# Performance work log

Hardware: AMD Instinct MI355X
Metric: run time of the kernel (lower is better)

The kernel has to match this reference:

```python
import jax, jax.numpy as jnp
import numpy as np

B, L, D, H, DK = 2, 1024, 1024, 16, 64
LN_EPS = 1e-5


def setup_inputs() -> dict:
    key = jax.random.key(0)
    ks = jax.random.split(key, 4)
    x = jax.random.normal(ks[0], (B, L, D), dtype=jnp.float32)
    W_qkv = jax.random.normal(ks[1], (D, 3 * D), dtype=jnp.float32) * 0.02
    W_o = jax.random.normal(ks[2], (D, D), dtype=jnp.float32) * 0.02
    W_LTM = jax.random.normal(ks[3], (H, DK, DK), dtype=jnp.float32) * 0.5
    return {
        "x": x,
        "W_qkv": W_qkv,
        "W_o": W_o,
        "W_LTM": W_LTM,
        "V_gs": jnp.zeros((H,), jnp.float32),
        "V_T0": jnp.zeros((H,), jnp.float32),
        "beta_tau": jnp.ones((H,), jnp.float32),
        "beta_gm": jnp.ones((H,), jnp.float32) * 0.1,
        "C_ch": jnp.ones((H,), jnp.float32),
        "gamma": jnp.ones((H,), jnp.float32) * 0.1,
        "alpha_ppd": jnp.ones((1,), jnp.float32),
        "IC_threshold": jnp.ones((1,), jnp.float32),
        "gate": jnp.zeros((H,), jnp.float32),
    }


def _stp_physics(W_LTM, V_gs, V_T0, beta_tau, beta_gm, C_ch, alpha_ppd, IC_threshold):
    # per-head params broadcast to (H, dk, dk)
    V_eff = V_gs[:, None, None] - V_T0[:, None, None] + W_LTM  # U_T = 1.0
    sp = jax.nn.softplus(V_eff)
    g_ch = beta_tau[:, None, None] * sp
    retention = jnp.exp(-g_ch / C_ch[:, None, None])  # = 1 - Lambda
    G = beta_gm[:, None, None] * sp * jax.nn.sigmoid(V_eff)
    sign_mask = jnp.tanh(alpha_ppd * (g_ch - IC_threshold))
    return retention, G, sign_mask


def reference(x, W_qkv, W_o, W_LTM, V_gs, V_T0, beta_tau, beta_gm, C_ch,
              gamma, alpha_ppd, IC_threshold, gate):
    Bb, Ll, Dd = x.shape
    qkv = (x @ W_qkv).reshape(Bb, Ll, 3, H, DK)
    q, k, v = qkv[:, :, 0], qkv[:, :, 1], qkv[:, :, 2]  # (B,L,H,dk)

    # LayerNorm over dk, no affine
    mu = jnp.mean(k, axis=-1, keepdims=True)
    var = jnp.var(k, axis=-1, keepdims=True)
    k_normed = (k - mu) * jax.lax.rsqrt(var + LN_EPS)

    # ---- causal softmax attention ----
    scale = 1.0 / np.sqrt(DK)
    attn = jnp.einsum('bihd,bjhd->bhij', q, k) * scale
    causal = jnp.tril(jnp.ones((Ll, Ll), dtype=bool))
    attn = jnp.where(causal[None, None], attn, -jnp.inf)
    attn = jax.nn.softmax(attn, axis=-1)
    softmax_out = jnp.einsum('bhij,bjhd->bihd', attn, v)  # (B,L,H,dk)

    # ---- STP fast-weight recurrence ----
    retention, G, sign_mask = _stp_physics(W_LTM, V_gs, V_T0, beta_tau,
                                           beta_gm, C_ch, alpha_ppd, IC_threshold)
    coeff = gamma[:, None, None] * sign_mask * G  # (H,dk,dk)

    def step(F_state, qkv_t):
        q_t, k_t, v_t = qkv_t  # (B,H,dk) each; k_t is normed
        hebbian = jnp.einsum('bhd,bhe->bhde', v_t, k_t)
        F_new = retention[None] * F_state + coeff[None] * hebbian
        y_t = jnp.einsum('bhde,bhe->bhd', W_LTM[None] + F_new, q_t)
        return F_new, y_t

    xs = (jnp.moveaxis(q, 1, 0), jnp.moveaxis(k_normed, 1, 0), jnp.moveaxis(v, 1, 0))
    F0 = jnp.zeros((Bb, H, DK, DK), dtype=x.dtype)
    _, ys = jax.lax.scan(step, F0, xs)
    stp_out = jnp.moveaxis(ys, 0, 1)  # (B,L,H,dk)

    g = jax.nn.sigmoid(gate)[None, None, :, None]
    y = g * softmax_out + (1.0 - g) * stp_out
    y = y.reshape(Bb, Ll, Dd)
    return y @ W_o
```

## Files before the change

kernel.cpp:

```cpp
#include <hip/hip_runtime.h>
#include <hip/hip_bf16.h>
#include <math.h>

#define LQ 1024
#define DH 1024
#define NH 16
#define DKH 64

typedef __bf16 bf16x8 __attribute__((ext_vector_type(8)));
typedef float f32x4 __attribute__((ext_vector_type(4)));
typedef const unsigned int __attribute__((address_space(1)))* gas1_t;
typedef unsigned int __attribute__((address_space(3)))* las3_t;

__device__ __forceinline__ unsigned pack2bf(float a, float b) {
  union { __hip_bfloat16 h[2]; unsigned u; } t;
  t.h[0] = __float2bfloat16(a);
  t.h[1] = __float2bfloat16(b);
  return t.u;
}
__device__ __forceinline__ void store_c(float* p, float v) { *p = v; }
__device__ __forceinline__ void store_c(__hip_bfloat16* p, float v) { *p = __float2bfloat16(v); }

__global__ __launch_bounds__(256) void physics_kernel(
    const float* __restrict__ W_LTM, const float* __restrict__ V_gs, const float* __restrict__ V_T0,
    const float* __restrict__ beta_tau, const float* __restrict__ beta_gm, const float* __restrict__ C_ch,
    const float* __restrict__ gamma_, const float* __restrict__ alpha_ppd, const float* __restrict__ IC_thr,
    const float* __restrict__ gate, float* __restrict__ ret, float* __restrict__ ret64,
    float* __restrict__ co, float* __restrict__ g_out) {
  int idx = blockIdx.x * 256 + threadIdx.x;
  int h = idx >> 12;
  float w = W_LTM[idx];
  float veff = V_gs[h] - V_T0[h] + w;
  float sp = fmaxf(veff, 0.f) + log1pf(expf(-fabsf(veff)));
  float gch = beta_tau[h] * sp;
  float e1 = gch / C_ch[h];
  float retv = expf(-e1);
  float sig = 1.f / (1.f + expf(-veff));
  float G = beta_gm[h] * sp * sig;
  float sm = tanhf(alpha_ppd[0] * (gch - IC_thr[0]));
  ret[idx] = retv;
  ret64[idx] = expf(-64.f * e1);
  co[idx] = gamma_[h] * sm * G;
  if (idx < NH) g_out[idx] = 1.f / (1.f + expf(-gate[idx]));
}

__global__ __launch_bounds__(256) void cvt_kernel(const float* __restrict__ in, __hip_bfloat16* __restrict__ out) {
  size_t i = (size_t)(blockIdx.x * 256 + threadIdx.x) * 4;
  float4 v = *(const float4*)(in + i);
  __hip_bfloat16 t[4] = {__float2bfloat16(v.x), __float2bfloat16(v.y),
                         __float2bfloat16(v.z), __float2bfloat16(v.w)};
  *(uint2*)(out + i) = *(uint2*)t;
}

__global__ __launch_bounds__(256) void tcvt_kernel(const float* __restrict__ W, __hip_bfloat16* __restrict__ Wt,
                                                   int K, int N) {
  __shared__ float t[32][33];
  int n0 = blockIdx.x * 32, k0 = blockIdx.y * 32;
  int r = threadIdx.x >> 5, c = threadIdx.x & 31;
#pragma unroll
  for (int i = 0; i < 4; i++) t[r + 8 * i][c] = W[(size_t)(k0 + r + 8 * i) * N + n0 + c];
  __syncthreads();
#pragma unroll
  for (int i = 0; i < 4; i++)
    Wt[(size_t)(n0 + r + 8 * i) * K + k0 + c] = __float2bfloat16(t[c][r + 8 * i]);
}

__global__ __launch_bounds__(256) void mix_kernel(const float* __restrict__ so, const float* __restrict__ stp,
                                                  const float* __restrict__ g, __hip_bfloat16* __restrict__ out) {
  size_t base = (size_t)(blockIdx.x * 256 + threadIdx.x) * 4;
  float gv = g[(base >> 6) & 15];
  float4 a = *(const float4*)(so + base);
  float4 b = *(const float4*)(stp + base);
  __hip_bfloat16 t[4] = {__float2bfloat16(gv * a.x + (1.f - gv) * b.x),
                         __float2bfloat16(gv * a.y + (1.f - gv) * b.y),
                         __float2bfloat16(gv * a.z + (1.f - gv) * b.z),
                         __float2bfloat16(gv * a.w + (1.f - gv) * b.w)};
  *(uint2*)(out + base) = *(uint2*)t;
}

template <typename OT>
__global__ __launch_bounds__(256) void gemm_bt_kernel(
    const __hip_bfloat16* __restrict__ A, const __hip_bfloat16* __restrict__ Bt,
    OT* __restrict__ C, int M, int N, int K) {
  __shared__ unsigned short As[128 * 32];
  __shared__ unsigned short Bs[128 * 32];
  const int tid = threadIdx.x;
  const int w = tid >> 6, lane = tid & 63;
  const int quad = lane >> 4, l16 = lane & 15;
  const int wm = w & 1, wn = w >> 1;
  const int row0 = blockIdx.y * 128, col0 = blockIdx.x * 128;
  const int sr = lane >> 2;
  const int sk = (lane & 3) * 8;
  f32x4 acc[4][4];
#pragma unroll
  for (int i = 0; i < 4; i++)
#pragma unroll
    for (int j = 0; j < 4; j++) acc[i][j] = (f32x4){0.f, 0.f, 0.f, 0.f};

  for (int k0 = 0; k0 < K; k0 += 32) {
    __syncthreads();
#pragma unroll
    for (int c = 0; c < 2; c++) {
      int s = c * 4 + w;
      const __hip_bfloat16* gA = A + (size_t)(row0 + s * 16 + sr) * K + k0 + sk;
      __builtin_amdgcn_global_load_lds((gas1_t)gA, (las3_t)((char*)As + s * 1024), 16, 0, 0);
      const __hip_bfloat16* gB = Bt + (size_t)(col0 + s * 16 + sr) * K + k0 + sk;
      __builtin_amdgcn_global_load_lds((gas1_t)gB, (las3_t)((char*)Bs + s * 1024), 16, 0, 0);
    }
    __syncthreads();
    bf16x8 af[4], bfr[4];
#pragma unroll
    for (int i = 0; i < 4; i++)
      af[i] = *(const bf16x8*)((const char*)As + (((wm * 64 + i * 16 + l16) * 32 + quad * 8) << 1));
#pragma unroll
    for (int j = 0; j < 4; j++)
      bfr[j] = *(const bf16x8*)((const char*)Bs + (((wn * 64 + j * 16 + l16) * 32 + quad * 8) << 1));
#pragma unroll
    for (int i = 0; i < 4; i++)
#pragma unroll
      for (int j = 0; j < 4; j++)
        acc[i][j] = __builtin_amdgcn_mfma_f32_16x16x32_bf16(af[i], bfr[j], acc[i][j], 0, 0, 0);
  }
#pragma unroll
  for (int i = 0; i < 4; i++) {
    int rowb = row0 + wm * 64 + i * 16 + quad * 4;
#pragma unroll
    for (int j = 0; j < 4; j++) {
      int col = col0 + wn * 64 + j * 16 + l16;
#pragma unroll
      for (int r = 0; r < 4; r++)
        store_c(&C[(size_t)(rowb + r) * N + col], acc[i][j][r]);
    }
  }
}

__global__ __launch_bounds__(256) void cvt_qkv_kernel(
    const __hip_bfloat16* __restrict__ qkvb, __hip_bfloat16* __restrict__ vt, float* __restrict__ kn) {
  const int tc = blockIdx.x, h = blockIdx.y, b = blockIdx.z;
  const int bh = b * NH + h;
  const int tid = threadIdx.x;
  const int r = tid >> 2;
  const int q4 = tid & 3;
  const int t = tc * 64 + r;
  __shared__ float Ls[64][65];
  const size_t rowbase = (size_t)(b * LQ + t) * 3 * DH + h * DKH + q4 * 16;

  {
    bf16x8 k0 = *(const bf16x8*)(qkvb + rowbase + DH);
    bf16x8 k1 = *(const bf16x8*)(qkvb + rowbase + DH + 8);
    float vv[16];
#pragma unroll
    for (int i = 0; i < 8; i++) { vv[i] = (float)k0[i]; vv[8 + i] = (float)k1[i]; }
    float s1 = 0.f, s2 = 0.f;
#pragma unroll
    for (int i = 0; i < 16; i++) { s1 += vv[i]; s2 += vv[i] * vv[i]; }
    s1 += __shfl_xor(s1, 1); s2 += __shfl_xor(s2, 1);
    s1 += __shfl_xor(s1, 2); s2 += __shfl_xor(s2, 2);
    float mu = s1 * (1.f / 64.f);
    float var = s2 * (1.f / 64.f) - mu * mu;
    float inv = rsqrtf(var + 1e-5f);
    float* kdst = kn + ((size_t)(b * LQ + t) * NH + h) * DKH + q4 * 16;
#pragma unroll
    for (int i4 = 0; i4 < 4; i4++) {
      float4 c = {(vv[i4 * 4] - mu) * inv, (vv[i4 * 4 + 1] - mu) * inv,
                  (vv[i4 * 4 + 2] - mu) * inv, (vv[i4 * 4 + 3] - mu) * inv};
      *(float4*)(kdst + i4 * 4) = c;
    }
  }
  {
    bf16x8 v0 = *(const bf16x8*)(qkvb + rowbase + 2 * DH);
    bf16x8 v1 = *(const bf16x8*)(qkvb + rowbase + 2 * DH + 8);
#pragma unroll
    for (int i = 0; i < 8; i++) {
      Ls[r][q4 * 16 + i] = (float)v0[i];
      Ls[r][q4 * 16 + 8 + i] = (float)v1[i];
    }
  }
  __syncthreads();
  {
    const int dr = tid >> 2, tq = tid & 3;
    __hip_bfloat16 o[16];
#pragma unroll
    for (int i = 0; i < 16; i++) o[i] = __float2bfloat16(Ls[tq * 16 + i][dr]);
    __hip_bfloat16* dst = vt + ((size_t)bh * DKH + dr) * LQ + tc * 64 + tq * 16;
    *(uint4*)dst = *(uint4*)o;
    *(uint4*)(dst + 8) = *(uint4*)(o + 8);
  }
}

__global__ __launch_bounds__(256) void attn_mfma_kernel(
    const __hip_bfloat16* __restrict__ qkvb, const __hip_bfloat16* __restrict__ vt,
    float* __restrict__ so) {
  const int it = 15 - blockIdx.x;
  const int h = blockIdx.y, b = blockIdx.z;
  const int bh = b * NH + h;
  const int tid = threadIdx.x;
  const int w = tid >> 6, lane = tid & 63;
  const int l16 = lane & 15, quad = lane >> 4;
  __shared__ __attribute__((aligned(16))) __hip_bfloat16 Ks[8 * 64 * 8];
  __shared__ __attribute__((aligned(16))) __hip_bfloat16 Vs[8 * 64 * 8];
  const int i0 = it * 64;
  const int q_abs = i0 + w * 16 + l16;
  bf16x8 aq[2];
  aq[0] = *(const bf16x8*)(qkvb + (size_t)(b * LQ + q_abs) * 3 * DH + h * DKH + quad * 8);
  aq[1] = *(const bf16x8*)(qkvb + (size_t)(b * LQ + q_abs) * 3 * DH + h * DKH + 32 + quad * 8);
  f32x4 o[4];
#pragma unroll
  for (int dt = 0; dt < 4; dt++) o[dt] = (f32x4){0.f, 0.f, 0.f, 0.f};
  float mrun = -3e38f, lrun = 0.f;

  for (int jt = 0; jt <= it; jt++) {
    const int j0 = jt * 64;
    __syncthreads();
#pragma unroll
    for (int ff = 0; ff < 2; ff++) {
      const int f = w * 2 + ff;
      const int nt = f >> 1, kk = f & 1;
      const __hip_bfloat16* gk = qkvb + (size_t)(b * LQ + j0 + nt * 16 + l16) * 3 * DH + DH +
                                 h * DKH + kk * 32 + quad * 8;
      __builtin_amdgcn_global_load_lds((gas1_t)gk, (las3_t)(Ks + f * 512), 16, 0, 0);
      const __hip_bfloat16* gv = vt + ((size_t)bh * DKH + nt * 16 + l16) * LQ + j0 + kk * 32 + quad * 8;
      __builtin_amdgcn_global_load_lds((gas1_t)gv, (las3_t)(Vs + f * 512), 16, 0, 0);
    }
    __syncthreads();
    f32x4 s[4];
#pragma unroll
    for (int nt = 0; nt < 4; nt++) s[nt] = (f32x4){0.f, 0.f, 0.f, 0.f};
#pragma unroll
    for (int kk = 0; kk < 2; kk++)
#pragma unroll
      for (int nt = 0; nt < 4; nt++) {
        bf16x8 bk = *(const bf16x8*)(Ks + ((nt * 2 + kk) * 64 + lane) * 8);
        s[nt] = __builtin_amdgcn_mfma_f32_16x16x32_bf16(bk, aq[kk], s[nt], 0, 0, 0);
      }
#pragma unroll
    for (int nt = 0; nt < 4; nt++)
#pragma unroll
      for (int r = 0; r < 4; r++) {
        float sv = s[nt][r] * 0.125f;
        if (jt == it && (j0 + nt * 16 + quad * 4 + r > q_abs)) sv = -1e30f;
        s[nt][r] = sv;
      }
    float mx = -3e38f;
#pragma unroll
    for (int nt = 0; nt < 4; nt++)
#pragma unroll
      for (int r = 0; r < 4; r++) mx = fmaxf(mx, s[nt][r]);
    mx = fmaxf(mx, __shfl_xor(mx, 16));
    mx = fmaxf(mx, __shfl_xor(mx, 32));
    float mn = fmaxf(mrun, mx);
    float al = __expf(mrun - mn);
    mrun = mn;
    float p[4][4];
    float rs = 0.f;
#pragma unroll
    for (int nt = 0; nt < 4; nt++)
#pragma unroll
      for (int r = 0; r < 4; r++) {
        float pv = __expf(s[nt][r] - mn);
        p[nt][r] = pv;
        rs += pv;
      }
    rs += __shfl_xor(rs, 16);
    rs += __shfl_xor(rs, 32);
    lrun = lrun * al + rs;
    unsigned pk[4][2];
#pragma unroll
    for (int nt = 0; nt < 4; nt++) {
      pk[nt][0] = pack2bf(p[nt][0], p[nt][1]);
      pk[nt][1] = pack2bf(p[nt][2], p[nt][3]);
    }
    const int srcA = l16 | ((quad & 1) << 5);
    const bool hi_sel = (quad >> 1) != 0;
    bf16x8 ap[2];
#pragma unroll
    for (int kk = 0; kk < 2; kk++) {
      union { unsigned u[4]; bf16x8 v; } cv;
#pragma unroll
      for (int g = 0; g < 2; g++) {
        int src = srcA + (g << 4);
        unsigned lo0 = (unsigned)__shfl((int)pk[kk * 2][0], src);
        unsigned lo1 = (unsigned)__shfl((int)pk[kk * 2][1], src);
        unsigned hi0 = (unsigned)__shfl((int)pk[kk * 2 + 1][0], src);
        unsigned hi1 = (unsigned)__shfl((int)pk[kk * 2 + 1][1], src);
        cv.u[g * 2] = hi_sel ? hi0 : lo0;
        cv.u[g * 2 + 1] = hi_sel ? hi1 : lo1;
      }
      ap[kk] = cv.v;
    }
#pragma unroll
    for (int dt = 0; dt < 4; dt++)
#pragma unroll
      for (int r = 0; r < 4; r++) o[dt][r] *= al;
#pragma unroll
    for (int kk = 0; kk < 2; kk++)
#pragma unroll
      for (int dt = 0; dt < 4; dt++) {
        bf16x8 bv = *(const bf16x8*)(Vs + ((dt * 2 + kk) * 64 + lane) * 8);
        o[dt] = __builtin_amdgcn_mfma_f32_16x16x32_bf16(bv, ap[kk], o[dt], 0, 0, 0);
      }
  }
  float inv = 1.f / lrun;
  float* ob = so + ((size_t)(b * LQ + q_abs) * NH + h) * DKH + quad * 4;
#pragma unroll
  for (int dt = 0; dt < 4; dt++) {
    float4 c = {o[dt][0] * inv, o[dt][1] * inv, o[dt][2] * inv, o[dt][3] * inv};
    *(float4*)(ob + dt * 16) = c;
  }
}

__global__ __launch_bounds__(256) void state_kernel(
    const __hip_bfloat16* __restrict__ qkvb, const float* __restrict__ kn,
    const float* __restrict__ ret_g, const float* __restrict__ co_g, float* __restrict__ S) {
  const int bh = blockIdx.x >> 1;
  const int half = blockIdx.x & 1;
  const int c = blockIdx.y;
  const int bb = bh >> 4, h = bh & 15;
  const int tid = threadIdx.x;
  const int dl = tid >> 3, j = tid & 7;
  const int d = half * 32 + dl;
  float F[8], R[8], Cc[8];
  const int base = h * 4096 + d * 64 + j * 8;
#pragma unroll
  for (int i = 0; i < 8; i++) {
    F[i] = 0.f;
    R[i] = ret_g[base + i];
    Cc[i] = co_g[base + i];
  }
  __shared__ float kb[2][8][64], vb[2][8][64];
  const int t00 = c * 64;
  {
    float ld[4];
#pragma unroll
    for (int i = 0; i < 4; i++) {
      int idx = tid + 256 * i;
      int which = idx >> 9, rem = idx & 511, s = rem >> 6, e = rem & 63;
      int t = t00 + s;
      if (which == 0) ld[i] = kn[((size_t)(bb * LQ + t) * NH + h) * DKH + e];
      else            ld[i] = __bfloat162float(qkvb[((size_t)(bb * LQ + t) * 3 + 2) * DH + h * DKH + e]);
    }
#pragma unroll
    for (int i = 0; i < 4; i++) {
      int idx = tid + 256 * i;
      int which = idx >> 9, rem = idx & 511, s = rem >> 6, e = rem & 63;
      if (which == 0) kb[0][s][e] = ld[i];
      else            vb[0][s][e] = ld[i];
    }
  }
  __syncthreads();
  for (int sc = 0; sc < 8; sc++) {
    const int p = sc & 1;
    float l2[4];
    if (sc < 7) {
      int t0 = t00 + (sc + 1) * 8;
#pragma unroll
      for (int i = 0; i < 4; i++) {
        int idx = tid + 256 * i;
        int which = idx >> 9, rem = idx & 511, s = rem >> 6, e = rem & 63;
        int t = t0 + s;
        if (which == 0) l2[i] = kn[((size_t)(bb * LQ + t) * NH + h) * DKH + e];
        else            l2[i] = __bfloat162float(qkvb[((size_t)(bb * LQ + t) * 3 + 2) * DH + h * DKH + e]);
      }
    }
#pragma unroll
    for (int s = 0; s < 8; s++) {
      float vd = vb[p][s][d];
#pragma unroll
      for (int i = 0; i < 8; i++) {
        float ke = kb[p][s][j * 8 + i];
        F[i] = fmaf(Cc[i] * vd, ke, R[i] * F[i]);
      }
    }
    if (sc < 7) {
      const int pn = p ^ 1;
#pragma unroll
      for (int i = 0; i < 4; i++) {
        int idx = tid + 256 * i;
        int which = idx >> 9, rem = idx & 511, s = rem >> 6, e = rem & 63;
        if (which == 0) kb[pn][s][e] = l2[i];
        else            vb[pn][s][e] = l2[i];
      }
    }
    __syncthreads();
  }
  const size_t sb = ((size_t)c * 2048 + ((size_t)bb * 16 + h) * 64 + d) * 64 + j * 8;
#pragma unroll
  for (int i = 0; i < 8; i++) S[sb + i] = F[i];
}

__global__ __launch_bounds__(256) void combine_kernel(
    const float* __restrict__ S, const float* __restrict__ ret64, float* __restrict__ Fs) {
  int n = blockIdx.x * 256 + threadIdx.x;
  float r64 = ret64[n & 65535];
  float F = 0.f;
  Fs[n] = 0.f;
#pragma unroll
  for (int c = 1; c < 16; c++) {
    F = fmaf(r64, F, S[(size_t)(c - 1) * 131072 + n]);
    Fs[(size_t)c * 131072 + n] = F;
  }
}

__global__ __launch_bounds__(256) void scan_out_kernel(
    const __hip_bfloat16* __restrict__ qkvb, const float* __restrict__ kn, const float* __restrict__ W_LTM,
    const float* __restrict__ ret_g, const float* __restrict__ co_g, const float* __restrict__ Fs,
    float* __restrict__ stp) {
  const int bh = blockIdx.x >> 1;
  const int half = blockIdx.x & 1;
  const int c = blockIdx.y;
  const int bb = bh >> 4, h = bh & 15;
  const int tid = threadIdx.x;
  const int dl = tid >> 3, j = tid & 7;
  const int d = half * 32 + dl;
  float F[8], R[8], Cc[8], W[8];
  const int base = h * 4096 + d * 64 + j * 8;
  const size_t nbase = (size_t)c * 131072 + (((size_t)bb * 16 + h) * 64 + d) * 64 + j * 8;
#pragma unroll
  for (int i = 0; i < 8; i++) {
    F[i] = Fs[nbase + i];
    R[i] = ret_g[base + i];
    Cc[i] = co_g[base + i];
    W[i] = W_LTM[base + i];
  }
  __shared__ float qb[2][8][64], kb[2][8][64], vb[2][8][64];
  const int t00 = c * 64;
  {
    float ld[6];
#pragma unroll
    for (int i = 0; i < 6; i++) {
      int idx = tid + 256 * i;
      int which = idx >> 9, rem = idx & 511, s = rem >> 6, e = rem & 63;
      int t = t00 + s;
      if (which == 0)      ld[i] = __bfloat162float(qkvb[((size_t)(bb * LQ + t) * 3 + 0) * DH + h * DKH + e]);
      else if (which == 1) ld[i] = kn[((size_t)(bb * LQ + t) * NH + h) * DKH + e];
      else                 ld[i] = __bfloat162float(qkvb[((size_t)(bb * LQ + t) * 3 + 2) * DH + h * DKH + e]);
    }
#pragma unroll
    for (int i = 0; i < 6; i++) {
      int idx = tid + 256 * i;
      int which = idx >> 9, rem = idx & 511, s = rem >> 6, e = rem & 63;
      if (which == 0) qb[0][s][e] = ld[i];
      else if (which == 1) kb[0][s][e] = ld[i];
      else vb[0][s][e] = ld[i];
    }
  }
  __syncthreads();
  for (int sc = 0; sc < 8; sc++) {
    const int p = sc & 1;
    float l2[6];
    if (sc < 7) {
      int t0 = t00 + (sc + 1) * 8;
#pragma unroll
      for (int i = 0; i < 6; i++) {
        int idx = tid + 256 * i;
        int which = idx >> 9, rem = idx & 511, s = rem >> 6, e = rem & 63;
        int t = t0 + s;
        if (which == 0)      l2[i] = __bfloat162float(qkvb[((size_t)(bb * LQ + t) * 3 + 0) * DH + h * DKH + e]);
        else if (which == 1) l2[i] = kn[((size_t)(bb * LQ + t) * NH + h) * DKH + e];
        else                 l2[i] = __bfloat162float(qkvb[((size_t)(bb * LQ + t) * 3 + 2) * DH + h * DKH + e]);
      }
    }
#pragma unroll
    for (int s = 0; s < 8; s++) {
      float vd = vb[p][s][d];
      float yp = 0.f;
#pragma unroll
      for (int i = 0; i < 8; i++) {
        float ke = kb[p][s][j * 8 + i];
        F[i] = fmaf(Cc[i] * vd, ke, R[i] * F[i]);
        yp = fmaf(W[i] + F[i], qb[p][s][j * 8 + i], yp);
      }
      yp += __shfl_xor(yp, 1);
      yp += __shfl_xor(yp, 2);
      yp += __shfl_xor(yp, 4);
      if (j == 0) stp[((size_t)(bb * LQ + t00 + sc * 8 + s) * NH + h) * DKH + d] = yp;
    }
    if (sc < 7) {
      const int pn = p ^ 1;
#pragma unroll
      for (int i = 0; i < 6; i++) {
        int idx = tid + 256 * i;
        int which = idx >> 9, rem = idx & 511, s = rem >> 6, e = rem & 63;
        if (which == 0) qb[pn][s][e] = l2[i];
        else if (which == 1) kb[pn][s][e] = l2[i];
        else vb[pn][s][e] = l2[i];
      }
    }
    __syncthreads();
  }
}

extern "C" void kernel_launch(void* const* d_in, const int* in_sizes, int n_in,
                              void* d_out, int out_size, void* d_ws, size_t ws_size,
                              hipStream_t stream) {
  (void)in_sizes; (void)n_in; (void)out_size; (void)ws_size;
  const float* x        = (const float*)d_in[0];
  const float* W_qkv    = (const float*)d_in[1];
  const float* W_o      = (const float*)d_in[2];
  const float* W_LTM    = (const float*)d_in[3];
  const float* V_gs     = (const float*)d_in[4];
  const float* V_T0     = (const float*)d_in[5];
  const float* beta_tau = (const float*)d_in[6];
  const float* beta_gm  = (const float*)d_in[7];
  const float* C_ch     = (const float*)d_in[8];
  const float* gamma_   = (const float*)d_in[9];
  const float* alpha_p  = (const float*)d_in[10];
  const float* IC_thr   = (const float*)d_in[11];
  const float* gate     = (const float*)d_in[12];

  float* ws  = (float*)d_ws;
  __hip_bfloat16* qkvb = (__hip_bfloat16*)ws;
  float* kn    = ws + 3145728;
  float* so    = kn + 2097152;
  float* stp   = so + 2097152;
  float* ret   = stp + 2097152;
  float* ret64 = ret + 65536;
  float* co    = ret64 + 65536;
  float* g     = co + 65536;
  __hip_bfloat16* xb  = (__hip_bfloat16*)(g + 64);
  __hip_bfloat16* wot = xb + 2097152;
  float* Sbuf = (float*)(wot + 1048576);
  float* Fs   = Sbuf + 1966080;
  __hip_bfloat16* vtb = (__hip_bfloat16*)(Fs + 2097152);
  __hip_bfloat16* mixb = xb;
  __hip_bfloat16* wqt  = (__hip_bfloat16*)stp;
  float* out = (float*)d_out;

  physics_kernel<<<256, 256, 0, stream>>>(W_LTM, V_gs, V_T0, beta_tau, beta_gm, C_ch,
                                          gamma_, alpha_p, IC_thr, gate, ret, ret64, co, g);
  cvt_kernel<<<2048, 256, 0, stream>>>(x, xb);
  tcvt_kernel<<<dim3(96, 32), 256, 0, stream>>>(W_qkv, wqt, 1024, 3072);
  tcvt_kernel<<<dim3(32, 32), 256, 0, stream>>>(W_o, wot, 1024, 1024);
  gemm_bt_kernel<__hip_bfloat16><<<dim3(24, 16), 256, 0, stream>>>(xb, wqt, qkvb, 2048, 3072, 1024);
  cvt_qkv_kernel<<<dim3(16, 16, 2), 256, 0, stream>>>(qkvb, vtb, kn);
  attn_mfma_kernel<<<dim3(16, 16, 2), 256, 0, stream>>>(qkvb, vtb, so);
  state_kernel<<<dim3(64, 15), 256, 0, stream>>>(qkvb, kn, ret, co, Sbuf);
  combine_kernel<<<512, 256, 0, stream>>>(Sbuf, ret64, Fs);
  scan_out_kernel<<<dim3(64, 16), 256, 0, stream>>>(qkvb, kn, W_LTM, ret, co, Fs, stp);
  mix_kernel<<<2048, 256, 0, stream>>>(so, stp, g, mixb);
  gemm_bt_kernel<float><<<dim3(8, 16), 256, 0, stream>>>(mixb, wot, out, 2048, 1024, 1024);
}
```

Before: 241.0 us.

## Fuse prep kernels, fold mix into scan, halve scan chunks, store bf16 intermediates

```diff
diff --git a/kernel.cpp b/kernel.cpp
--- a/kernel.cpp
+++ b/kernel.cpp
@@ -21,61 +21,58 @@
 __device__ __forceinline__ void store_c(float* p, float v) { *p = v; }
 __device__ __forceinline__ void store_c(__hip_bfloat16* p, float v) { *p = __float2bfloat16(v); }
 
-__global__ __launch_bounds__(256) void physics_kernel(
+__global__ __launch_bounds__(256) void prep_kernel(
+    const float* __restrict__ x, const float* __restrict__ W_qkv, const float* __restrict__ W_o,
     const float* __restrict__ W_LTM, const float* __restrict__ V_gs, const float* __restrict__ V_T0,
     const float* __restrict__ beta_tau, const float* __restrict__ beta_gm, const float* __restrict__ C_ch,
     const float* __restrict__ gamma_, const float* __restrict__ alpha_ppd, const float* __restrict__ IC_thr,
-    const float* __restrict__ gate, float* __restrict__ ret, float* __restrict__ ret64,
-    float* __restrict__ co, float* __restrict__ g_out) {
-  int idx = blockIdx.x * 256 + threadIdx.x;
-  int h = idx >> 12;
-  float w = W_LTM[idx];
-  float veff = V_gs[h] - V_T0[h] + w;
-  float sp = fmaxf(veff, 0.f) + log1pf(expf(-fabsf(veff)));
-  float gch = beta_tau[h] * sp;
-  float e1 = gch / C_ch[h];
-  float retv = expf(-e1);
-  float sig = 1.f / (1.f + expf(-veff));
-  float G = beta_gm[h] * sp * sig;
-  float sm = tanhf(alpha_ppd[0] * (gch - IC_thr[0]));
-  ret[idx] = retv;
-  ret64[idx] = expf(-64.f * e1);
-  co[idx] = gamma_[h] * sm * G;
-  if (idx < NH) g_out[idx] = 1.f / (1.f + expf(-gate[idx]));
-}
-
-__global__ __launch_bounds__(256) void cvt_kernel(const float* __restrict__ in, __hip_bfloat16* __restrict__ out) {
-  size_t i = (size_t)(blockIdx.x * 256 + threadIdx.x) * 4;
-  float4 v = *(const float4*)(in + i);
-  __hip_bfloat16 t[4] = {__float2bfloat16(v.x), __float2bfloat16(v.y),
-                         __float2bfloat16(v.z), __float2bfloat16(v.w)};
-  *(uint2*)(out + i) = *(uint2*)t;
-}
-
-__global__ __launch_bounds__(256) void tcvt_kernel(const float* __restrict__ W, __hip_bfloat16* __restrict__ Wt,
-                                                   int K, int N) {
-  __shared__ float t[32][33];
-  int n0 = blockIdx.x * 32, k0 = blockIdx.y * 32;
-  int r = threadIdx.x >> 5, c = threadIdx.x & 31;
-#pragma unroll
-  for (int i = 0; i < 4; i++) t[r + 8 * i][c] = W[(size_t)(k0 + r + 8 * i) * N + n0 + c];
-  __syncthreads();
-#pragma unroll
-  for (int i = 0; i < 4; i++)
-    Wt[(size_t)(n0 + r + 8 * i) * K + k0 + c] = __float2bfloat16(t[c][r + 8 * i]);
-}
-
-__global__ __launch_bounds__(256) void mix_kernel(const float* __restrict__ so, const float* __restrict__ stp,
-                                                  const float* __restrict__ g, __hip_bfloat16* __restrict__ out) {
-  size_t base = (size_t)(blockIdx.x * 256 + threadIdx.x) * 4;
-  float gv = g[(base >> 6) & 15];
-  float4 a = *(const float4*)(so + base);
-  float4 b = *(const float4*)(stp + base);
-  __hip_bfloat16 t[4] = {__float2bfloat16(gv * a.x + (1.f - gv) * b.x),
-                         __float2bfloat16(gv * a.y + (1.f - gv) * b.y),
-                         __float2bfloat16(gv * a.z + (1.f - gv) * b.z),
-                         __float2bfloat16(gv * a.w + (1.f - gv) * b.w)};
-  *(uint2*)(out + base) = *(uint2*)t;
+    const float* __restrict__ gate,
+    __hip_bfloat16* __restrict__ xb, __hip_bfloat16* __restrict__ wqt, __hip_bfloat16* __restrict__ wot,
+    float* __restrict__ ret, float* __restrict__ ret32, float* __restrict__ co, float* __restrict__ g_out) {
+  __shared__ float ts[32][33];
+  const int bx = blockIdx.x, tid = threadIdx.x;
+  if (bx < 256) {
+    int idx = bx * 256 + tid;
+    int h = idx >> 12;
+    float w = W_LTM[idx];
+    float veff = V_gs[h] - V_T0[h] + w;
+    float sp = fmaxf(veff, 0.f) + log1pf(expf(-fabsf(veff)));
+    float gch = beta_tau[h] * sp;
+    float e1 = gch / C_ch[h];
+    float sig = 1.f / (1.f + expf(-veff));
+    float G = beta_gm[h] * sp * sig;
+    float sm = tanhf(alpha_ppd[0] * (gch - IC_thr[0]));
+    ret[idx] = expf(-e1);
+    ret32[idx] = expf(-32.f * e1);
+    co[idx] = gamma_[h] * sm * G;
+    if (idx < NH) g_out[idx] = 1.f / (1.f + expf(-gate[idx]));
+  } else if (bx < 2304) {
+    size_t i = (size_t)((bx - 256) * 256 + tid) * 4;
+    float4 v = *(const float4*)(x + i);
+    __hip_bfloat16 t[4] = {__float2bfloat16(v.x), __float2bfloat16(v.y),
+                           __float2bfloat16(v.z), __float2bfloat16(v.w)};
+    *(uint2*)(xb + i) = *(uint2*)t;
+  } else {
+    const float* W;
+    __hip_bfloat16* Wt;
+    int n0, k0, N;
+    if (bx < 5376) {
+      int idx = bx - 2304;
+      W = W_qkv; Wt = wqt; N = 3072;
+      n0 = (idx % 96) * 32; k0 = (idx / 96) * 32;
+    } else {
+      int idx = bx - 5376;
+      W = W_o; Wt = wot; N = 1024;
+      n0 = (idx & 31) * 32; k0 = (idx >> 5) * 32;
+    }
+    int r = tid >> 5, c = tid & 31;
+#pragma unroll
+    for (int i = 0; i < 4; i++) ts[r + 8 * i][c] = W[(size_t)(k0 + r + 8 * i) * N + n0 + c];
+    __syncthreads();
+#pragma unroll
+    for (int i = 0; i < 4; i++)
+      Wt[(size_t)(n0 + r + 8 * i) * 1024 + k0 + c] = __float2bfloat16(ts[c][r + 8 * i]);
+  }
 }
 
 template <typename OT>
@@ -135,7 +132,8 @@
 }
 
 __global__ __launch_bounds__(256) void cvt_qkv_kernel(
-    const __hip_bfloat16* __restrict__ qkvb, __hip_bfloat16* __restrict__ vt, float* __restrict__ kn) {
+    const __hip_bfloat16* __restrict__ qkvb, __hip_bfloat16* __restrict__ vt,
+    __hip_bfloat16* __restrict__ knb) {
   const int tc = blockIdx.x, h = blockIdx.y, b = blockIdx.z;
   const int bh = b * NH + h;
   const int tid = threadIdx.x;
@@ -159,13 +157,12 @@
     float mu = s1 * (1.f / 64.f);
     float var = s2 * (1.f / 64.f) - mu * mu;
     float inv = rsqrtf(var + 1e-5f);
-    float* kdst = kn + ((size_t)(b * LQ + t) * NH + h) * DKH + q4 * 16;
-#pragma unroll
-    for (int i4 = 0; i4 < 4; i4++) {
-      float4 c = {(vv[i4 * 4] - mu) * inv, (vv[i4 * 4 + 1] - mu) * inv,
-                  (vv[i4 * 4 + 2] - mu) * inv, (vv[i4 * 4 + 3] - mu) * inv};
-      *(float4*)(kdst + i4 * 4) = c;
-    }
+    __hip_bfloat16 ko[16];
+#pragma unroll
+    for (int i = 0; i < 16; i++) ko[i] = __float2bfloat16((vv[i] - mu) * inv);
+    __hip_bfloat16* kdst = knb + ((size_t)(b * LQ + t) * NH + h) * DKH + q4 * 16;
+    *(uint4*)kdst = *(uint4*)ko;
+    *(uint4*)(kdst + 8) = *(uint4*)(ko + 8);
   }
   {
     bf16x8 v0 = *(const bf16x8*)(qkvb + rowbase + 2 * DH);
@@ -190,7 +187,7 @@
 
 __global__ __launch_bounds__(256) void attn_mfma_kernel(
     const __hip_bfloat16* __restrict__ qkvb, const __hip_bfloat16* __restrict__ vt,
-    float* __restrict__ so) {
+    __hip_bfloat16* __restrict__ sob) {
   const int it = 15 - blockIdx.x;
   const int h = blockIdx.y, b = blockIdx.z;
   const int bh = b * NH + h;
@@ -301,16 +298,17 @@
       }
   }
   float inv = 1.f / lrun;
-  float* ob = so + ((size_t)(b * LQ + q_abs) * NH + h) * DKH + quad * 4;
+  __hip_bfloat16* ob = sob + ((size_t)(b * LQ + q_abs) * NH + h) * DKH + quad * 4;
 #pragma unroll
   for (int dt = 0; dt < 4; dt++) {
-    float4 c = {o[dt][0] * inv, o[dt][1] * inv, o[dt][2] * inv, o[dt][3] * inv};
-    *(float4*)(ob + dt * 16) = c;
+    uint2 val = {pack2bf(o[dt][0] * inv, o[dt][1] * inv),
+                 pack2bf(o[dt][2] * inv, o[dt][3] * inv)};
+    *(uint2*)(ob + dt * 16) = val;
   }
 }
 
 __global__ __launch_bounds__(256) void state_kernel(
-    const __hip_bfloat16* __restrict__ qkvb, const float* __restrict__ kn,
+    const __hip_bfloat16* __restrict__ qkvb, const __hip_bfloat16* __restrict__ knb,
     const float* __restrict__ ret_g, const float* __restrict__ co_g, float* __restrict__ S) {
   const int bh = blockIdx.x >> 1;
   const int half = blockIdx.x & 1;
@@ -328,7 +326,7 @@
     Cc[i] = co_g[base + i];
   }
   __shared__ float kb[2][8][64], vb[2][8][64];
-  const int t00 = c * 64;
+  const int t00 = c * 32;
   {
     float ld[4];
 #pragma unroll
@@ -336,7 +334,7 @@
       int idx = tid + 256 * i;
       int which = idx >> 9, rem = idx & 511, s = rem >> 6, e = rem & 63;
       int t = t00 + s;
-      if (which == 0) ld[i] = kn[((size_t)(bb * LQ + t) * NH + h) * DKH + e];
+      if (which == 0) ld[i] = __bfloat162float(knb[((size_t)(bb * LQ + t) * NH + h) * DKH + e]);
       else            ld[i] = __bfloat162float(qkvb[((size_t)(bb * LQ + t) * 3 + 2) * DH + h * DKH + e]);
     }
 #pragma unroll
@@ -348,17 +346,17 @@
     }
   }
   __syncthreads();
-  for (int sc = 0; sc < 8; sc++) {
+  for (int sc = 0; sc < 4; sc++) {
     const int p = sc & 1;
     float l2[4];
-    if (sc < 7) {
+    if (sc < 3) {
       int t0 = t00 + (sc + 1) * 8;
 #pragma unroll
       for (int i = 0; i < 4; i++) {
         int idx = tid + 256 * i;
         int which = idx >> 9, rem = idx & 511, s = rem >> 6, e = rem & 63;
         int t = t0 + s;
-        if (which == 0) l2[i] = kn[((size_t)(bb * LQ + t) * NH + h) * DKH + e];
+        if (which == 0) l2[i] = __bfloat162float(knb[((size_t)(bb * LQ + t) * NH + h) * DKH + e]);
         else            l2[i] = __bfloat162float(qkvb[((size_t)(bb * LQ + t) * 3 + 2) * DH + h * DKH + e]);
       }
     }
@@ -371,7 +369,7 @@
         F[i] = fmaf(Cc[i] * vd, ke, R[i] * F[i]);
       }
     }
-    if (sc < 7) {
+    if (sc < 3) {
       const int pn = p ^ 1;
 #pragma unroll
       for (int i = 0; i < 4; i++) {
@@ -389,22 +387,23 @@
 }
 
 __global__ __launch_bounds__(256) void combine_kernel(
-    const float* __restrict__ S, const float* __restrict__ ret64, float* __restrict__ Fs) {
+    const float* __restrict__ S, const float* __restrict__ ret32, float* __restrict__ Fs) {
   int n = blockIdx.x * 256 + threadIdx.x;
-  float r64 = ret64[n & 65535];
+  float r32 = ret32[n & 65535];
   float F = 0.f;
   Fs[n] = 0.f;
 #pragma unroll
-  for (int c = 1; c < 16; c++) {
-    F = fmaf(r64, F, S[(size_t)(c - 1) * 131072 + n]);
+  for (int c = 1; c < 32; c++) {
+    F = fmaf(r32, F, S[(size_t)(c - 1) * 131072 + n]);
     Fs[(size_t)c * 131072 + n] = F;
   }
 }
 
 __global__ __launch_bounds__(256) void scan_out_kernel(
-    const __hip_bfloat16* __restrict__ qkvb, const float* __restrict__ kn, const float* __restrict__ W_LTM,
-    const float* __restrict__ ret_g, const float* __restrict__ co_g, const float* __restrict__ Fs,
-    float* __restrict__ stp) {
+    const __hip_bfloat16* __restrict__ qkvb, const __hip_bfloat16* __restrict__ knb,
+    const float* __restrict__ W_LTM, const float* __restrict__ ret_g, const float* __restrict__ co_g,
+    const float* __restrict__ Fs, const __hip_bfloat16* __restrict__ sob,
+    const float* __restrict__ g, __hip_bfloat16* __restrict__ mixb) {
   const int bh = blockIdx.x >> 1;
   const int half = blockIdx.x & 1;
   const int c = blockIdx.y;
@@ -412,6 +411,7 @@
   const int tid = threadIdx.x;
   const int dl = tid >> 3, j = tid & 7;
   const int d = half * 32 + dl;
+  const float gh = g[h];
   float F[8], R[8], Cc[8], W[8];
   const int base = h * 4096 + d * 64 + j * 8;
   const size_t nbase = (size_t)c * 131072 + (((size_t)bb * 16 + h) * 64 + d) * 64 + j * 8;
@@ -423,7 +423,7 @@
     W[i] = W_LTM[base + i];
   }
   __shared__ float qb[2][8][64], kb[2][8][64], vb[2][8][64];
-  const int t00 = c * 64;
+  const int t00 = c * 32;
   {
     float ld[6];
 #pragma unroll
@@ -432,7 +432,7 @@
       int which = idx >> 9, rem = idx & 511, s = rem >> 6, e = rem & 63;
       int t = t00 + s;
       if (which == 0)      ld[i] = __bfloat162float(qkvb[((size_t)(bb * LQ + t) * 3 + 0) * DH + h * DKH + e]);
-      else if (which == 1) ld[i] = kn[((size_t)(bb * LQ + t) * NH + h) * DKH + e];
+      else if (which == 1) ld[i] = __bfloat162float(knb[((size_t)(bb * LQ + t) * NH + h) * DKH + e]);
       else                 ld[i] = __bfloat162float(qkvb[((size_t)(bb * LQ + t) * 3 + 2) * DH + h * DKH + e]);
     }
 #pragma unroll
@@ -445,10 +445,10 @@
     }
   }
   __syncthreads();
-  for (int sc = 0; sc < 8; sc++) {
+  for (int sc = 0; sc < 4; sc++) {
     const int p = sc & 1;
     float l2[6];
-    if (sc < 7) {
+    if (sc < 3) {
       int t0 = t00 + (sc + 1) * 8;
 #pragma unroll
       for (int i = 0; i < 6; i++) {
@@ -456,7 +456,7 @@
         int which = idx >> 9, rem = idx & 511, s = rem >> 6, e = rem & 63;
         int t = t0 + s;
         if (which == 0)      l2[i] = __bfloat162float(qkvb[((size_t)(bb * LQ + t) * 3 + 0) * DH + h * DKH + e]);
-        else if (which == 1) l2[i] = kn[((size_t)(bb * LQ + t) * NH + h) * DKH + e];
+        else if (which == 1) l2[i] = __bfloat162float(knb[((size_t)(bb * LQ + t) * NH + h) * DKH + e]);
         else                 l2[i] = __bfloat162float(qkvb[((size_t)(bb * LQ + t) * 3 + 2) * DH + h * DKH + e]);
       }
     }
@@ -473,9 +473,13 @@
       yp += __shfl_xor(yp, 1);
       yp += __shfl_xor(yp, 2);
       yp += __shfl_xor(yp, 4);
-      if (j == 0) stp[((size_t)(bb * LQ + t00 + sc * 8 + s) * NH + h) * DKH + d] = yp;
-    }
-    if (sc < 7) {
+      if (j == 0) {
+        const size_t oi = ((size_t)(bb * LQ + t00 + sc * 8 + s) * NH + h) * DKH + d;
+        float sv = __bfloat162float(sob[oi]);
+        mixb[oi] = __float2bfloat16(gh * sv + (1.f - gh) * yp);
+      }
+    }
+    if (sc < 3) {
       const int pn = p ^ 1;
 #pragma unroll
       for (int i = 0; i < 6; i++) {
@@ -510,33 +514,29 @@
 
   float* ws  = (float*)d_ws;
   __hip_bfloat16* qkvb = (__hip_bfloat16*)ws;
-  float* kn    = ws + 3145728;
-  float* so    = kn + 2097152;
-  float* stp   = so + 2097152;
-  float* ret   = stp + 2097152;
-  float* ret64 = ret + 65536;
-  float* co    = ret64 + 65536;
+  __hip_bfloat16* knb  = (__hip_bfloat16*)(ws + 3145728);
+  __hip_bfloat16* sob  = (__hip_bfloat16*)(ws + 4194304);
+  __hip_bfloat16* mixb = (__hip_bfloat16*)(ws + 5242880);
+  __hip_bfloat16* vtb  = (__hip_bfloat16*)(ws + 6291456);
+  __hip_bfloat16* xb   = (__hip_bfloat16*)(ws + 7340032);
+  __hip_bfloat16* wqt  = (__hip_bfloat16*)(ws + 8388608);
+  __hip_bfloat16* wot  = (__hip_bfloat16*)(ws + 9961472);
+  float* ret   = ws + 10485760;
+  float* ret32 = ret + 65536;
+  float* co    = ret32 + 65536;
   float* g     = co + 65536;
-  __hip_bfloat16* xb  = (__hip_bfloat16*)(g + 64);
-  __hip_bfloat16* wot = xb + 2097152;
-  float* Sbuf = (float*)(wot + 1048576);
-  float* Fs   = Sbuf + 1966080;
-  __hip_bfloat16* vtb = (__hip_bfloat16*)(Fs + 2097152);
-  __hip_bfloat16* mixb = xb;
-  __hip_bfloat16* wqt  = (__hip_bfloat16*)stp;
+  float* Sbuf  = g + 64;
+  float* Fs    = Sbuf + 4063232;
   float* out = (float*)d_out;
 
-  physics_kernel<<<256, 256, 0, stream>>>(W_LTM, V_gs, V_T0, beta_tau, beta_gm, C_ch,
-                                          gamma_, alpha_p, IC_thr, gate, ret, ret64, co, g);
-  cvt_kernel<<<2048, 256, 0, stream>>>(x, xb);
-  tcvt_kernel<<<dim3(96, 32), 256, 0, stream>>>(W_qkv, wqt, 1024, 3072);
-  tcvt_kernel<<<dim3(32, 32), 256, 0, stream>>>(W_o, wot, 1024, 1024);
+  prep_kernel<<<6400, 256, 0, stream>>>(x, W_qkv, W_o, W_LTM, V_gs, V_T0, beta_tau, beta_gm,
+                                        C_ch, gamma_, alpha_p, IC_thr, gate,
+                                        xb, wqt, wot, ret, ret32, co, g);
   gemm_bt_kernel<__hip_bfloat16><<<dim3(24, 16), 256, 0, stream>>>(xb, wqt, qkvb, 2048, 3072, 1024);
-  cvt_qkv_kernel<<<dim3(16, 16, 2), 256, 0, stream>>>(qkvb, vtb, kn);
-  attn_mfma_kernel<<<dim3(16, 16, 2), 256, 0, stream>>>(qkvb, vtb, so);
-  state_kernel<<<dim3(64, 15), 256, 0, stream>>>(qkvb, kn, ret, co, Sbuf);
-  combine_kernel<<<512, 256, 0, stream>>>(Sbuf, ret64, Fs);
-  scan_out_kernel<<<dim3(64, 16), 256, 0, stream>>>(qkvb, kn, W_LTM, ret, co, Fs, stp);
-  mix_kernel<<<2048, 256, 0, stream>>>(so, stp, g, mixb);
+  cvt_qkv_kernel<<<dim3(16, 16, 2), 256, 0, stream>>>(qkvb, vtb, knb);
+  attn_mfma_kernel<<<dim3(16, 16, 2), 256, 0, stream>>>(qkvb, vtb, sob);
+  state_kernel<<<dim3(64, 31), 256, 0, stream>>>(qkvb, knb, ret, co, Sbuf);
+  combine_kernel<<<512, 256, 0, stream>>>(Sbuf, ret32, Fs);
+  scan_out_kernel<<<dim3(64, 32), 256, 0, stream>>>(qkvb, knb, W_LTM, ret, co, Fs, sob, g, mixb);
   gemm_bt_kernel<float><<<dim3(8, 16), 256, 0, stream>>>(mixb, wot, out, 2048, 1024, 1024);
 }
```

Measured after the change: 246.3 us. 2.2% more time.
